# Kernel tuning notes

Hardware: AMD Instinct MI355X
Metric: run time of the kernel (lower is better)

The kernel has to match this reference:

```python
import jax, jax.numpy as jnp
import numpy as np

# column-index constants for the node feature matrix and edge attributes
VM, VA, PG, QG, PD, QD = 0, 1, 2, 3, 4, 5
G_COL, B_COL = 0, 1

N_NODES = 100000
N_EDGES = 3200000
N_FEAT = 6


def setup_inputs() -> dict:
    key = jax.random.key(0)
    k1, k2, k3, k4, k5, k6 = jax.random.split(key, 6)
    pred = jax.random.normal(k1, (N_NODES, N_FEAT), dtype=jnp.float32)
    target = jax.random.normal(k2, (N_NODES, N_FEAT), dtype=jnp.float32)
    src = jax.random.randint(k3, (N_EDGES,), 0, N_NODES, dtype=jnp.int32)
    dst = jax.random.randint(k4, (N_EDGES,), 0, N_NODES, dtype=jnp.int32)
    edge_index = jnp.stack([src, dst], axis=0)
    edge_attr = jax.random.normal(k5, (N_EDGES, 2), dtype=jnp.float32)
    mask = jax.random.bernoulli(k6, 0.5, (N_NODES, N_FEAT))
    return {"pred": pred, "target": target, "edge_index": edge_index,
            "edge_attr": edge_attr, "mask": mask}


def reference(pred, target, edge_index, edge_attr, mask):
    # temp_pred[~mask] = target[~mask]
    tp = jnp.where(mask, pred, target)

    V_m = tp[:, VM]
    V_a = tp[:, VA]
    V = V_m * jnp.exp(1j * V_a)           # complex64 [N]
    V_conj = jnp.conj(V)

    # conj(Y_bus) entries on edges: G - jB
    Y_conj = edge_attr[:, G_COL] - 1j * edge_attr[:, B_COL]  # complex64 [E]

    row, col = edge_index[0], edge_index[1]
    # (Y_bus_conj @ V_conj)[i] = sum over edges (i,j) of conj(Y_ij) * conj(V_j)
    msg = Y_conj * V_conj[col]                               # gather-multiply [E]
    matvec = jax.ops.segment_sum(msg, row, num_segments=tp.shape[0])  # scatter-add [N]

    S_injection = V * matvec                                  # diag(V) @ (...)

    net_P = tp[:, PG] - tp[:, PD]
    net_Q = tp[:, QG] - tp[:, QD]
    diff = (net_P + 1j * net_Q) - S_injection

    loss = jnp.mean(jnp.abs(diff))
    real_loss = jnp.mean(jnp.abs(jnp.real(diff)))
    imag_loss = jnp.mean(jnp.abs(jnp.imag(diff)))
    return (loss, real_loss, imag_loss)
```

## Files before the change

### kernel.cpp

```cpp
#include <hip/hip_runtime.h>
#include <hip/hip_fp16.h>
#include <math.h>

constexpr int N_NODES = 100000;
constexpr int N_EDGES = 3200000;
constexpr int NF      = 6;

constexpr int BSHIFT  = 10;
constexpr int BNODES  = 1 << BSHIFT;
constexpr int NB      = (N_NODES + BNODES - 1) >> BSHIFT;
constexpr int CAP     = 33792;
constexpr int TILE    = 2048;
constexpr int EPT     = TILE / 256;
constexpr int NBLK_PART = (N_EDGES + TILE - 1) / TILE;
constexpr int VPREP_BLOCKS = (N_NODES + 255) / 256;

constexpr size_t OFF_V    = 0;
constexpr size_t OFF_REC  = OFF_V + (size_t)N_NODES * 8;
constexpr size_t OFF_CNT  = OFF_REC + (size_t)NB * CAP * 8;
constexpr size_t WS_NEED  = OFF_CNT + 1024;

__device__ __forceinline__ float2 half2u_to_f2(unsigned u) {
    __half2 h;
    *reinterpret_cast<unsigned*>(&h) = u;
    return __half22float2(h);
}

__global__ __launch_bounds__(256) void partition_edges(
        const int* __restrict__ row, const int* __restrict__ col,
        const float2* __restrict__ attr,
        const float* __restrict__ pred, const float* __restrict__ target,
        const unsigned char* __restrict__ mask,
        float2* __restrict__ v_out,
        unsigned int* __restrict__ gcur,
        uint2* __restrict__ rec_g) {
    __shared__ unsigned int h[4][NB];
    __shared__ unsigned int cur[4][NB];
    __shared__ int wb[4][NB];
    __shared__ int dbase[NB];
    __shared__ unsigned int tot_s[NB];
    __shared__ uint2 rec_s[TILE];
    __shared__ unsigned char bkt_s[TILE];
    __shared__ int total_s;

    const int tid = threadIdx.x;
    const int w = tid >> 6;
    const int e0 = blockIdx.x * TILE;
    const int e_base = e0 + tid * EPT;
    const bool ok = e_base < N_EDGES;

    if (blockIdx.x < VPREP_BLOCKS) {
        int i = blockIdx.x * 256 + tid;
        if (i < N_NODES) {
            const int bb = i * NF;
            float vm = mask[bb + 0] ? pred[bb + 0] : target[bb + 0];
            float va = mask[bb + 1] ? pred[bb + 1] : target[bb + 1];
            float sn, cs;
            sincosf(va, &sn, &cs);
            v_out[i] = make_float2(vm * cs, vm * sn);
        }
    }

    for (int i = tid; i < 4 * NB; i += 256) {
        (&h[0][0])[i] = 0u;
        (&cur[0][0])[i] = 0u;
    }
    __syncthreads();

    int r[EPT];
    if (ok) {
        int4 ra = *(const int4*)(row + e_base);
        int4 rb = *(const int4*)(row + e_base + 4);
        r[0]=ra.x; r[1]=ra.y; r[2]=ra.z; r[3]=ra.w;
        r[4]=rb.x; r[5]=rb.y; r[6]=rb.z; r[7]=rb.w;
        #pragma unroll
        for (int k = 0; k < EPT; ++k)
            atomicAdd(&h[w][r[k] >> BSHIFT], 1u);
    }
    __syncthreads();

    if (tid < NB)
        tot_s[tid] = h[0][tid] + h[1][tid] + h[2][tid] + h[3][tid];
    __syncthreads();

    if (tid < NB) {
        int lbase = 0;
        for (int j = 0; j < tid; ++j) lbase += (int)tot_s[j];
        unsigned t0 = h[0][tid], t1 = h[1][tid], t2 = h[2][tid];
        unsigned tot = tot_s[tid];
        unsigned g = tot ? atomicAdd(&gcur[tid], tot) : 0u;
        dbase[tid] = (int)g - lbase;
        wb[0][tid] = lbase;
        wb[1][tid] = lbase + (int)t0;
        wb[2][tid] = lbase + (int)(t0 + t1);
        wb[3][tid] = lbase + (int)(t0 + t1 + t2);
        if (tid == NB - 1) total_s = lbase + (int)tot;
    }
    __syncthreads();

    if (ok) {
        int4 ca = *(const int4*)(col + e_base);
        int4 cb = *(const int4*)(col + e_base + 4);
        int c[EPT] = {ca.x, ca.y, ca.z, ca.w, cb.x, cb.y, cb.z, cb.w};
        float4 a0 = *(const float4*)(attr + e_base);
        float4 a1 = *(const float4*)(attr + e_base + 2);
        float4 a2 = *(const float4*)(attr + e_base + 4);
        float4 a3 = *(const float4*)(attr + e_base + 6);
        float gx[EPT] = {a0.x, a0.z, a1.x, a1.z, a2.x, a2.z, a3.x, a3.z};
        float gy[EPT] = {a0.y, a0.w, a1.y, a1.w, a2.y, a2.w, a3.y, a3.w};
        #pragma unroll
        for (int k = 0; k < EPT; ++k) {
            int rr = r[k];
            int b = rr >> BSHIFT;
            int slot = wb[w][b] + (int)atomicAdd(&cur[w][b], 1u);
            __half2 hh = __floats2half2_rn(gx[k], gy[k]);
            rec_s[slot] = make_uint2(
                (unsigned)c[k] | ((unsigned)(rr & (BNODES - 1)) << 17),
                *reinterpret_cast<unsigned int*>(&hh));
            bkt_s[slot] = (unsigned char)b;
        }
    }
    __syncthreads();

    const int total = total_s;
    for (int j = tid; j < total; j += 256) {
        int b = (int)bkt_s[j];
        int g = dbase[b] + j;
        if (g < CAP)
            rec_g[(size_t)b * CAP + g] = rec_s[j];
    }
}

__global__ __launch_bounds__(1024) void accum_bucket(
        const unsigned int* __restrict__ gcur,
        const uint2* __restrict__ rec,
        const float2* __restrict__ v,
        const float* __restrict__ pred,
        const float* __restrict__ target,
        const unsigned char* __restrict__ mask,
        float* __restrict__ sums,
        unsigned int* __restrict__ done_all,
        float* __restrict__ out) {
    __shared__ float acc_re[BNODES];
    __shared__ float acc_im[BNODES];
    const int tid = threadIdx.x;
    const int b = blockIdx.x;
    const int cnt = (int)min(gcur[b], (unsigned)CAP);
    acc_re[tid] = 0.f;
    acc_im[tid] = 0.f;
    __syncthreads();
    const uint2* rp = rec + (size_t)b * CAP;
    int j = 4 * tid;
    for (; j + 3 < cnt; j += 4 * BNODES) {
        uint4 q0 = *(const uint4*)(rp + j);
        uint4 q1 = *(const uint4*)(rp + j + 2);
        int c0 = (int)(q0.x & 0x1FFFFu), li0 = (int)(q0.x >> 17);
        int c1 = (int)(q0.z & 0x1FFFFu), li1 = (int)(q0.z >> 17);
        int c2 = (int)(q1.x & 0x1FFFFu), li2 = (int)(q1.x >> 17);
        int c3 = (int)(q1.z & 0x1FFFFu), li3 = (int)(q1.z >> 17);
        float2 vv0 = v[c0];
        float2 vv1 = v[c1];
        float2 vv2 = v[c2];
        float2 vv3 = v[c3];
        float2 gb0 = half2u_to_f2(q0.y);
        float2 gb1 = half2u_to_f2(q0.w);
        float2 gb2 = half2u_to_f2(q1.y);
        float2 gb3 = half2u_to_f2(q1.w);
        atomicAdd(&acc_re[li0], fmaf(gb0.x, vv0.x, -gb0.y * vv0.y));
        atomicAdd(&acc_im[li0], -fmaf(gb0.x, vv0.y, gb0.y * vv0.x));
        atomicAdd(&acc_re[li1], fmaf(gb1.x, vv1.x, -gb1.y * vv1.y));
        atomicAdd(&acc_im[li1], -fmaf(gb1.x, vv1.y, gb1.y * vv1.x));
        atomicAdd(&acc_re[li2], fmaf(gb2.x, vv2.x, -gb2.y * vv2.y));
        atomicAdd(&acc_im[li2], -fmaf(gb2.x, vv2.y, gb2.y * vv2.x));
        atomicAdd(&acc_re[li3], fmaf(gb3.x, vv3.x, -gb3.y * vv3.y));
        atomicAdd(&acc_im[li3], -fmaf(gb3.x, vv3.y, gb3.y * vv3.x));
    }
    for (; j < cnt; ++j) {
        uint2 q = rp[j];
        int c0 = (int)(q.x & 0x1FFFFu), li0 = (int)(q.x >> 17);
        float2 vv0 = v[c0];
        float2 gb0 = half2u_to_f2(q.y);
        atomicAdd(&acc_re[li0], fmaf(gb0.x, vv0.x, -gb0.y * vv0.y));
        atomicAdd(&acc_im[li0], -fmaf(gb0.x, vv0.y, gb0.y * vv0.x));
    }
    __syncthreads();

    float a = 0.f, ar = 0.f, ai = 0.f;
    {
        int i = (b << BSHIFT) + tid;
        if (i < N_NODES) {
            float mr = acc_re[tid];
            float mi = acc_im[tid];
            const int bb = i * NF;
            uchar2 m23 = *(const uchar2*)(mask + bb + 2);
            uchar2 m45 = *(const uchar2*)(mask + bb + 4);
            float2 p23 = *(const float2*)(pred + bb + 2);
            float2 p45 = *(const float2*)(pred + bb + 4);
            float2 t23 = *(const float2*)(target + bb + 2);
            float2 t45 = *(const float2*)(target + bb + 4);
            float pg = m23.x ? p23.x : t23.x;
            float qg = m23.y ? p23.y : t23.y;
            float pd = m45.x ? p45.x : t45.x;
            float qd = m45.y ? p45.y : t45.y;
            float2 vv = v[i];
            float s_re = vv.x * mr - vv.y * mi;
            float s_im = vv.x * mi + vv.y * mr;
            float dre = (pg - pd) - s_re;
            float dim = (qg - qd) - s_im;
            ar = fabsf(dre);
            ai = fabsf(dim);
            a  = sqrtf(dre * dre + dim * dim);
        }
    }
    #pragma unroll
    for (int off = 32; off > 0; off >>= 1) {
        a  += __shfl_down(a,  off, 64);
        ar += __shfl_down(ar, off, 64);
        ai += __shfl_down(ai, off, 64);
    }
    __shared__ float red[3][16];
    int wave = tid >> 6;
    int lane = tid & 63;
    if (lane == 0) { red[0][wave] = a; red[1][wave] = ar; red[2][wave] = ai; }
    __syncthreads();
    if (tid == 0) {
        float s0 = 0.f, s1 = 0.f, s2 = 0.f;
        #pragma unroll
        for (int k = 0; k < 16; ++k) { s0 += red[0][k]; s1 += red[1][k]; s2 += red[2][k]; }
        float r0 = atomicAdd(&sums[0], s0);
        float r1 = atomicAdd(&sums[1], s1);
        float r2 = atomicAdd(&sums[2], s2);
        float chk = r0 + r1 + r2;
        if (chk == chk) {
            unsigned fin = atomicAdd(done_all, 1u);
            if (fin == (unsigned)(NB - 1)) {
                const float inv = 1.0f / (float)N_NODES;
                float t0 = atomicAdd(&sums[0], 0.f);
                float t1 = atomicAdd(&sums[1], 0.f);
                float t2 = atomicAdd(&sums[2], 0.f);
                __hip_atomic_store(&out[0], t0 * inv, __ATOMIC_RELAXED, __HIP_MEMORY_SCOPE_AGENT);
                __hip_atomic_store(&out[1], t1 * inv, __ATOMIC_RELAXED, __HIP_MEMORY_SCOPE_AGENT);
                __hip_atomic_store(&out[2], t2 * inv, __ATOMIC_RELAXED, __HIP_MEMORY_SCOPE_AGENT);
            }
        }
    }
}

__global__ void node_prep_fb(const float* __restrict__ pred,
                             const float* __restrict__ target,
                             const unsigned char* __restrict__ mask,
                             float2* __restrict__ v) {
    int i = blockIdx.x * blockDim.x + threadIdx.x;
    if (i >= N_NODES) return;
    const int b = i * NF;
    float vm = mask[b + 0] ? pred[b + 0] : target[b + 0];
    float va = mask[b + 1] ? pred[b + 1] : target[b + 1];
    float s, c;
    sincosf(va, &s, &c);
    v[i] = make_float2(vm * c, vm * s);
}

__global__ void edge_scatter_fb(const int* __restrict__ row,
                                const int* __restrict__ col,
                                const float2* __restrict__ attr,
                                const float2* __restrict__ v,
                                float2* __restrict__ mv) {
    int e = blockIdx.x * blockDim.x + threadIdx.x;
    if (e >= N_EDGES) return;
    int r = row[e];
    int c = col[e];
    float2 gb = attr[e];
    float2 vv = v[c];
    float mre = fmaf(gb.x, vv.x, -gb.y * vv.y);
    float mim = -fmaf(gb.x, vv.y, gb.y * vv.x);
    atomicAdd(&mv[r].x, mre);
    atomicAdd(&mv[r].y, mim);
}

__global__ void finalize_fb(const float* __restrict__ pred,
                            const float* __restrict__ target,
                            const unsigned char* __restrict__ mask,
                            const float2* __restrict__ v,
                            const float2* __restrict__ mv,
                            float* __restrict__ sums) {
    int i = blockIdx.x * blockDim.x + threadIdx.x;
    float a = 0.f, ar = 0.f, ai = 0.f;
    if (i < N_NODES) {
        const int b = i * NF;
        float pg = mask[b + 2] ? pred[b + 2] : target[b + 2];
        float qg = mask[b + 3] ? pred[b + 3] : target[b + 3];
        float pd = mask[b + 4] ? pred[b + 4] : target[b + 4];
        float qd = mask[b + 5] ? pred[b + 5] : target[b + 5];
        float netP = pg - pd;
        float netQ = qg - qd;
        float2 vv = v[i];
        float2 m = mv[i];
        float s_re = vv.x * m.x - vv.y * m.y;
        float s_im = vv.x * m.y + vv.y * m.x;
        float dre = netP - s_re;
        float dim = netQ - s_im;
        ar = fabsf(dre);
        ai = fabsf(dim);
        a  = sqrtf(dre * dre + dim * dim);
    }
    #pragma unroll
    for (int off = 32; off > 0; off >>= 1) {
        a  += __shfl_down(a,  off, 64);
        ar += __shfl_down(ar, off, 64);
        ai += __shfl_down(ai, off, 64);
    }
    __shared__ float red[3][4];
    int wave = threadIdx.x >> 6;
    int lane = threadIdx.x & 63;
    if (lane == 0) { red[0][wave] = a; red[1][wave] = ar; red[2][wave] = ai; }
    __syncthreads();
    if (threadIdx.x == 0) {
        atomicAdd(&sums[0], red[0][0] + red[0][1] + red[0][2] + red[0][3]);
        atomicAdd(&sums[1], red[1][0] + red[1][1] + red[1][2] + red[1][3]);
        atomicAdd(&sums[2], red[2][0] + red[2][1] + red[2][2] + red[2][3]);
    }
}

__global__ void write_out_fb(const float* __restrict__ sums, float* __restrict__ out) {
    if (threadIdx.x == 0 && blockIdx.x == 0) {
        const float inv = 1.0f / (float)N_NODES;
        out[0] = sums[0] * inv;
        out[1] = sums[1] * inv;
        out[2] = sums[2] * inv;
    }
}

extern "C" void kernel_launch(void* const* d_in, const int* in_sizes, int n_in,
                              void* d_out, int out_size, void* d_ws, size_t ws_size,
                              hipStream_t stream) {
    const float*         pred   = (const float*)d_in[0];
    const float*         target = (const float*)d_in[1];
    const int*           eidx   = (const int*)d_in[2];
    const float2*        attr   = (const float2*)d_in[3];
    const unsigned char* mask   = (const unsigned char*)d_in[4];
    float* out = (float*)d_out;

    const int* row = eidx;
    const int* col = eidx + N_EDGES;

    char* ws = (char*)d_ws;
    const int B = 256;

    if (ws_size >= WS_NEED) {
        float2*       v        = (float2*)(ws + OFF_V);
        uint2*        rec_g    = (uint2*)(ws + OFF_REC);
        unsigned int* gcur     = (unsigned int*)(ws + OFF_CNT);
        float*        sums     = (float*)(ws + OFF_CNT + 912);
        unsigned int* done_all = (unsigned int*)(ws + OFF_CNT + 928);

        hipMemsetAsync(ws + OFF_CNT, 0, 1024, stream);
        partition_edges<<<NBLK_PART, B, 0, stream>>>(row, col, attr,
                                                     pred, target, mask, v,
                                                     gcur, rec_g);
        accum_bucket<<<NB, BNODES, 0, stream>>>(gcur, rec_g, v,
                                                pred, target, mask,
                                                sums, done_all, out);
    } else {
        float2* v    = (float2*)ws;
        float2* mv   = (float2*)(ws + (size_t)N_NODES * 8);
        float*  sums = (float*)(ws + 2ull * N_NODES * 8);
        hipMemsetAsync(mv, 0, (size_t)N_NODES * 8 + 16, stream);
        node_prep_fb<<<(N_NODES + B - 1) / B, B, 0, stream>>>(pred, target, mask, v);
        edge_scatter_fb<<<(N_EDGES + B - 1) / B, B, 0, stream>>>(row, col, attr, v, mv);
        finalize_fb<<<(N_NODES + B - 1) / B, B, 0, stream>>>(pred, target, mask, v, mv, sums);
        write_out_fb<<<1, 64, 0, stream>>>(sums, out);
    }
}
```

Before: 221.9 us.

## Repartition nodes into 256 near-equal buckets to fill all CUs

Replaces the 98 power-of-two node buckets of 1024 nodes with 256 buckets of about 391 nodes, assigned by a multiply-shift division. The goal is to launch one accumulate block per CU on the 256-CU device instead of leaving most CUs idle in the second kernel. In exchange it adds per-edge bucket arithmetic in the partition kernel and more histogram and cursor slots per partition block. The per-bucket record capacity is reduced to match, which risks overflow if edges are unevenly distributed.

```diff
diff --git a/kernel.cpp b/kernel.cpp
--- a/kernel.cpp
+++ b/kernel.cpp
@@ -6,19 +6,25 @@
 constexpr int N_EDGES = 3200000;
 constexpr int NF      = 6;
 
-constexpr int BSHIFT  = 10;
-constexpr int BNODES  = 1 << BSHIFT;
-constexpr int NB      = (N_NODES + BNODES - 1) >> BSHIFT;
-constexpr int CAP     = 33792;
+constexpr int NB      = 256;
+constexpr int NMAXB   = 392;
+constexpr int CAP     = 13312;
 constexpr int TILE    = 2048;
 constexpr int EPT     = TILE / 256;
 constexpr int NBLK_PART = (N_EDGES + TILE - 1) / TILE;
 constexpr int VPREP_BLOCKS = (N_NODES + 255) / 256;
 
+__device__ __forceinline__ unsigned bucket_of(int r) {
+    return (unsigned)(((unsigned long long)((unsigned)r << 8) * 351843721ull) >> 45);
+}
+__device__ __forceinline__ int base_of(unsigned b) {
+    return (int)((b * 100000u + 255u) >> 8);
+}
+
 constexpr size_t OFF_V    = 0;
 constexpr size_t OFF_REC  = OFF_V + (size_t)N_NODES * 8;
 constexpr size_t OFF_CNT  = OFF_REC + (size_t)NB * CAP * 8;
-constexpr size_t WS_NEED  = OFF_CNT + 1024;
+constexpr size_t WS_NEED  = OFF_CNT + 2048;
 
 __device__ __forceinline__ float2 half2u_to_f2(unsigned u) {
     __half2 h;
@@ -68,14 +74,17 @@
     __syncthreads();
 
     int r[EPT];
+    unsigned bk[EPT];
     if (ok) {
         int4 ra = *(const int4*)(row + e_base);
         int4 rb = *(const int4*)(row + e_base + 4);
         r[0]=ra.x; r[1]=ra.y; r[2]=ra.z; r[3]=ra.w;
         r[4]=rb.x; r[5]=rb.y; r[6]=rb.z; r[7]=rb.w;
         #pragma unroll
-        for (int k = 0; k < EPT; ++k)
-            atomicAdd(&h[w][r[k] >> BSHIFT], 1u);
+        for (int k = 0; k < EPT; ++k) {
+            bk[k] = bucket_of(r[k]);
+            atomicAdd(&h[w][bk[k]], 1u);
+        }
     }
     __syncthreads();
 
@@ -110,13 +119,12 @@
         float gy[EPT] = {a0.y, a0.w, a1.y, a1.w, a2.y, a2.w, a3.y, a3.w};
         #pragma unroll
         for (int k = 0; k < EPT; ++k) {
-            int rr = r[k];
-            int b = rr >> BSHIFT;
+            unsigned b = bk[k];
+            unsigned li = (unsigned)(r[k] - base_of(b));
             int slot = wb[w][b] + (int)atomicAdd(&cur[w][b], 1u);
             __half2 hh = __floats2half2_rn(gx[k], gy[k]);
-            rec_s[slot] = make_uint2(
-                (unsigned)c[k] | ((unsigned)(rr & (BNODES - 1)) << 17),
-                *reinterpret_cast<unsigned int*>(&hh));
+            rec_s[slot] = make_uint2((unsigned)c[k] | (li << 17),
+                                     *reinterpret_cast<unsigned int*>(&hh));
             bkt_s[slot] = (unsigned char)b;
         }
     }
@@ -141,17 +149,16 @@
         float* __restrict__ sums,
         unsigned int* __restrict__ done_all,
         float* __restrict__ out) {
-    __shared__ float acc_re[BNODES];
-    __shared__ float acc_im[BNODES];
+    __shared__ float acc_re[NMAXB];
+    __shared__ float acc_im[NMAXB];
     const int tid = threadIdx.x;
     const int b = blockIdx.x;
     const int cnt = (int)min(gcur[b], (unsigned)CAP);
-    acc_re[tid] = 0.f;
-    acc_im[tid] = 0.f;
+    if (tid < NMAXB) { acc_re[tid] = 0.f; acc_im[tid] = 0.f; }
     __syncthreads();
     const uint2* rp = rec + (size_t)b * CAP;
     int j = 4 * tid;
-    for (; j + 3 < cnt; j += 4 * BNODES) {
+    for (; j + 3 < cnt; j += 4096) {
         uint4 q0 = *(const uint4*)(rp + j);
         uint4 q1 = *(const uint4*)(rp + j + 2);
         int c0 = (int)(q0.x & 0x1FFFFu), li0 = (int)(q0.x >> 17);
@@ -185,32 +192,32 @@
     }
     __syncthreads();
 
+    const int base = base_of((unsigned)b);
+    const int nb_nodes = base_of((unsigned)b + 1) - base;
     float a = 0.f, ar = 0.f, ai = 0.f;
-    {
-        int i = (b << BSHIFT) + tid;
-        if (i < N_NODES) {
-            float mr = acc_re[tid];
-            float mi = acc_im[tid];
-            const int bb = i * NF;
-            uchar2 m23 = *(const uchar2*)(mask + bb + 2);
-            uchar2 m45 = *(const uchar2*)(mask + bb + 4);
-            float2 p23 = *(const float2*)(pred + bb + 2);
-            float2 p45 = *(const float2*)(pred + bb + 4);
-            float2 t23 = *(const float2*)(target + bb + 2);
-            float2 t45 = *(const float2*)(target + bb + 4);
-            float pg = m23.x ? p23.x : t23.x;
-            float qg = m23.y ? p23.y : t23.y;
-            float pd = m45.x ? p45.x : t45.x;
-            float qd = m45.y ? p45.y : t45.y;
-            float2 vv = v[i];
-            float s_re = vv.x * mr - vv.y * mi;
-            float s_im = vv.x * mi + vv.y * mr;
-            float dre = (pg - pd) - s_re;
-            float dim = (qg - qd) - s_im;
-            ar = fabsf(dre);
-            ai = fabsf(dim);
-            a  = sqrtf(dre * dre + dim * dim);
-        }
+    if (tid < nb_nodes) {
+        int i = base + tid;
+        float mr = acc_re[tid];
+        float mi = acc_im[tid];
+        const int bb = i * NF;
+        uchar2 m23 = *(const uchar2*)(mask + bb + 2);
+        uchar2 m45 = *(const uchar2*)(mask + bb + 4);
+        float2 p23 = *(const float2*)(pred + bb + 2);
+        float2 p45 = *(const float2*)(pred + bb + 4);
+        float2 t23 = *(const float2*)(target + bb + 2);
+        float2 t45 = *(const float2*)(target + bb + 4);
+        float pg = m23.x ? p23.x : t23.x;
+        float qg = m23.y ? p23.y : t23.y;
+        float pd = m45.x ? p45.x : t45.x;
+        float qd = m45.y ? p45.y : t45.y;
+        float2 vv = v[i];
+        float s_re = vv.x * mr - vv.y * mi;
+        float s_im = vv.x * mi + vv.y * mr;
+        float dre = (pg - pd) - s_re;
+        float dim = (qg - qd) - s_im;
+        ar = fabsf(dre);
+        ai = fabsf(dim);
+        a  = sqrtf(dre * dre + dim * dim);
     }
     #pragma unroll
     for (int off = 32; off > 0; off >>= 1) {
@@ -350,16 +357,16 @@
         float2*       v        = (float2*)(ws + OFF_V);
         uint2*        rec_g    = (uint2*)(ws + OFF_REC);
         unsigned int* gcur     = (unsigned int*)(ws + OFF_CNT);
-        float*        sums     = (float*)(ws + OFF_CNT + 912);
-        unsigned int* done_all = (unsigned int*)(ws + OFF_CNT + 928);
-
-        hipMemsetAsync(ws + OFF_CNT, 0, 1024, stream);
+        float*        sums     = (float*)(ws + OFF_CNT + 1536);
+        unsigned int* done_all = (unsigned int*)(ws + OFF_CNT + 1552);
+
+        hipMemsetAsync(ws + OFF_CNT, 0, 2048, stream);
         partition_edges<<<NBLK_PART, B, 0, stream>>>(row, col, attr,
                                                      pred, target, mask, v,
                                                      gcur, rec_g);
-        accum_bucket<<<NB, BNODES, 0, stream>>>(gcur, rec_g, v,
-                                                pred, target, mask,
-                                                sums, done_all, out);
+        accum_bucket<<<NB, 1024, 0, stream>>>(gcur, rec_g, v,
+                                              pred, target, mask,
+                                              sums, done_all, out);
     } else {
         float2* v    = (float2*)ws;
         float2* mv   = (float2*)(ws + (size_t)N_NODES * 8);
```

After: 178.1 us. 19.7% less time.
